# Performance work log

Hardware: AMD Instinct MI355X
Metric: run time of the kernel (lower is better)

## Reference

```python
import jax, jax.numpy as jnp
import numpy as np

NEG_SLOPE = 0.2


def gat_layer(x, src, dst, W, a_src, a_dst, b, heads, ch, concat, n_nodes):
    # x: [N, F_in], W: [F_in, heads*ch]
    h = (x @ W).reshape(n_nodes, heads, ch)              # [N, H, C]
    alpha_src = jnp.sum(h * a_src, axis=-1)              # [N, H]
    alpha_dst = jnp.sum(h * a_dst, axis=-1)              # [N, H]
    e = jax.nn.leaky_relu(alpha_src[src] + alpha_dst[dst], NEG_SLOPE)  # [E, H]
    # segment softmax over edges grouped by destination node
    e_max = jax.ops.segment_max(e, dst, num_segments=n_nodes)          # [N, H]
    ex = jnp.exp(e - e_max[dst])                                       # [E, H]
    denom = jax.ops.segment_sum(ex, dst, num_segments=n_nodes)         # [N, H]
    alpha = ex / denom[dst]                                            # [E, H]
    msg = h[src] * alpha[:, :, None]                                   # [E, H, C]
    out = jax.ops.segment_sum(msg, dst, num_segments=n_nodes)          # [N, H, C]
    if concat:
        out = out.reshape(n_nodes, heads * ch)
    else:
        out = out.mean(axis=1)
    return out + b


def setup_inputs() -> dict:
    key = jax.random.key(0)
    ks = jax.random.split(key, 16)
    N, E, F_in = 50000, 800000, 128
    H, C, OUT = 4, 32, 64
    x = jax.random.normal(ks[0], (N, F_in), dtype=jnp.float32)
    edge_index = jax.random.randint(ks[1], (2, E), 0, N, dtype=jnp.int64)
    s = 0.1
    return {
        "x": x,
        "edge_index": edge_index,
        "W1": jax.random.normal(ks[2], (F_in, H * C), dtype=jnp.float32) * s,
        "a_src1": jax.random.normal(ks[3], (H, C), dtype=jnp.float32) * s,
        "a_dst1": jax.random.normal(ks[4], (H, C), dtype=jnp.float32) * s,
        "b1": jnp.zeros((H * C,), dtype=jnp.float32),
        "W2": jax.random.normal(ks[5], (H * C, H * C), dtype=jnp.float32) * s,
        "a_src2": jax.random.normal(ks[6], (H, C), dtype=jnp.float32) * s,
        "a_dst2": jax.random.normal(ks[7], (H, C), dtype=jnp.float32) * s,
        "b2": jnp.zeros((H * C,), dtype=jnp.float32),
        "W3": jax.random.normal(ks[8], (H * C, H * OUT), dtype=jnp.float32) * s,
        "a_src3": jax.random.normal(ks[9], (H, OUT), dtype=jnp.float32) * s,
        "a_dst3": jax.random.normal(ks[10], (H, OUT), dtype=jnp.float32) * s,
        "b3": jnp.zeros((OUT,), dtype=jnp.float32),
    }


def reference(x, edge_index, W1, a_src1, a_dst1, b1, W2, a_src2, a_dst2, b2,
              W3, a_src3, a_dst3, b3):
    N = x.shape[0]
    # PyG GATConv default add_self_loops=True
    loop = jnp.arange(N, dtype=edge_index.dtype)
    src = jnp.concatenate([edge_index[0], loop])
    dst = jnp.concatenate([edge_index[1], loop])
    h = gat_layer(x, src, dst, W1, a_src1, a_dst1, b1, 4, 32, True, N)
    h = gat_layer(h, src, dst, W2, a_src2, a_dst2, b2, 4, 32, True, N)
    out = gat_layer(h, src, dst, W3, a_src3, a_dst3, b3, 4, 64, False, N)
    return out
```

## Files before the change

### kernel.cpp

```cpp
#include <hip/hip_runtime.h>
#include <hip/hip_fp16.h>

constexpr int HEADS = 4;

typedef _Float16 half8 __attribute__((ext_vector_type(8)));
typedef _Float16 half2v __attribute__((ext_vector_type(2)));
typedef float f32x4 __attribute__((ext_vector_type(4)));

__device__ __forceinline__ float lrelu(float x) { return x > 0.f ? x : 0.2f * x; }


__global__ void count_deg_kernel(const int* __restrict__ ei, int* __restrict__ deg,
                                 int E, int N) {
  int e = blockIdx.x * 256 + threadIdx.x;
  int EP = E + N;
  if (e < EP) {
    int d = (e < E) ? ei[E + e] : (e - E);
    atomicAdd(&deg[d], 1);
  }
}

__global__ void scan_block_kernel(const int* __restrict__ deg, int* __restrict__ rowp,
                                  int* __restrict__ partials, int N) {
  __shared__ int sm[1024];
  int t = threadIdx.x;
  int i = blockIdx.x * 1024 + t;
  int v = (i < N) ? deg[i] : 0;
  sm[t] = v;
  __syncthreads();
  for (int off = 1; off < 1024; off <<= 1) {
    int tmp = (t >= off) ? sm[t - off] : 0;
    __syncthreads();
    sm[t] += tmp;
    __syncthreads();
  }
  if (i < N) rowp[i] = sm[t] - v;
  if (t == 1023) partials[blockIdx.x] = sm[t];
}

__global__ void scan_partials_kernel(int* partials, int nb) {
  __shared__ int sm[1024];
  int t = threadIdx.x;
  int v = (t < nb) ? partials[t] : 0;
  sm[t] = v;
  __syncthreads();
  for (int off = 1; off < 1024; off <<= 1) {
    int tmp = (t >= off) ? sm[t - off] : 0;
    __syncthreads();
    sm[t] += tmp;
    __syncthreads();
  }
  if (t < nb) partials[t] = sm[t] - v;
}

__global__ void add_off_kernel(int* __restrict__ rowp, const int* __restrict__ partials,
                               int N, int EP) {
  int i = blockIdx.x * 256 + threadIdx.x;
  if (i < N) rowp[i] += partials[i >> 10];
  if (i == 0) rowp[N] = EP;
}

__global__ void scatter_kernel(const int* __restrict__ ei, const int* __restrict__ rowp,
                               int* __restrict__ cursor, int* __restrict__ col,
                               int* __restrict__ dstarr, int E, int N) {
  int e = blockIdx.x * 256 + threadIdx.x;
  int EP = E + N;
  if (e < EP) {
    int s, d;
    if (e < E) { s = ei[e]; d = ei[E + e]; }
    else       { s = e - E; d = e - E; }
    int pos = rowp[d] + atomicAdd(&cursor[d], 1);
    col[pos] = s;
    dstarr[pos] = d;
  }
}


__global__ void convert_wt3_kernel(const float* __restrict__ W1, _Float16* __restrict__ Wt1,
                                   const float* __restrict__ W2, _Float16* __restrict__ Wt2,
                                   const float* __restrict__ W3, _Float16* __restrict__ Wt3) {
  const float* W; _Float16* Wt; int Fout;
  if (blockIdx.y == 0)      { W = W1; Wt = Wt1; Fout = 128; }
  else if (blockIdx.y == 1) { W = W2; Wt = Wt2; Fout = 128; }
  else                      { W = W3; Wt = Wt3; Fout = 256; }
  int i = blockIdx.x * 256 + threadIdx.x;
  if (i < 128 * Fout) {
    int c = i >> 7, k = i & 127;
    Wt[c * 128 + k] = (_Float16)W[k * Fout + c];
  }
}


template <int AF32>
__global__ __launch_bounds__(256) void gemm_mfma_kernel(
    const void* __restrict__ Xv, const _Float16* __restrict__ Wt,
    _Float16* __restrict__ O, int N, int Fout) {
  const int w = threadIdx.x >> 6;
  const int lane = threadIdx.x & 63;
  const int r = lane & 15, g = lane >> 4;
  const int row0 = blockIdx.x * 64 + w * 16;
  const int colpan = blockIdx.y * 128;

  int rowl = row0 + r;
  if (rowl >= N) rowl = N - 1;

  f32x4 acc[8];
#pragma unroll
  for (int c = 0; c < 8; ++c) acc[c] = {0.f, 0.f, 0.f, 0.f};

#pragma unroll
  for (int s = 0; s < 4; ++s) {
    half8 a;
    if constexpr (AF32) {
      const float* X = (const float*)Xv;
      float4 a0 = *(const float4*)&X[(size_t)rowl * 128 + s * 32 + g * 8];
      float4 a1 = *(const float4*)&X[(size_t)rowl * 128 + s * 32 + g * 8 + 4];
      a = half8{(_Float16)a0.x, (_Float16)a0.y, (_Float16)a0.z, (_Float16)a0.w,
                (_Float16)a1.x, (_Float16)a1.y, (_Float16)a1.z, (_Float16)a1.w};
    } else {
      const _Float16* X = (const _Float16*)Xv;
      a = *(const half8*)&X[(size_t)rowl * 128 + s * 32 + g * 8];
    }
#pragma unroll
    for (int c = 0; c < 8; ++c) {
      half8 b = *(const half8*)&Wt[(size_t)(colpan + c * 16 + r) * 128 + s * 32 + g * 8];
      acc[c] = __builtin_amdgcn_mfma_f32_16x16x32_f16(a, b, acc[c], 0, 0, 0);
    }
  }

#pragma unroll
  for (int c = 0; c < 8; ++c) {
    int ocol = colpan + c * 16 + r;
#pragma unroll
    for (int q = 0; q < 4; ++q) {
      int orow = row0 + g * 4 + q;
      if (orow < N) O[(size_t)orow * Fout + ocol] = (_Float16)acc[c][q];
    }
  }
}


template <int LP>
__global__ __launch_bounds__(256) void alpha_kernel(
    const _Float16* __restrict__ H, const float* __restrict__ a_s,
    const float* __restrict__ a_d, float* __restrict__ asrc,
    float* __restrict__ adst, int N) {
  const int C = LP * 8;
  int g = blockIdx.x * 256 + threadIdx.x;
  int pair = g / LP;
  int sub = g % LP;
  if (pair >= N * 4) return;
  int h = pair & 3;
  half8 hv = *(const half8*)&H[(size_t)pair * C + sub * 8];
  float4 s0 = *(const float4*)&a_s[h * C + sub * 8];
  float4 s1 = *(const float4*)&a_s[h * C + sub * 8 + 4];
  float4 d0 = *(const float4*)&a_d[h * C + sub * 8];
  float4 d1 = *(const float4*)&a_d[h * C + sub * 8 + 4];
  float ps = (float)hv[0] * s0.x + (float)hv[1] * s0.y + (float)hv[2] * s0.z +
             (float)hv[3] * s0.w + (float)hv[4] * s1.x + (float)hv[5] * s1.y +
             (float)hv[6] * s1.z + (float)hv[7] * s1.w;
  float pd = (float)hv[0] * d0.x + (float)hv[1] * d0.y + (float)hv[2] * d0.z +
             (float)hv[3] * d0.w + (float)hv[4] * d1.x + (float)hv[5] * d1.y +
             (float)hv[6] * d1.z + (float)hv[7] * d1.w;
#pragma unroll
  for (int off = 1; off < LP; off <<= 1) {
    ps += __shfl_xor(ps, off, 64);
    pd += __shfl_xor(pd, off, 64);
  }
  if (sub == 0) { asrc[pair] = ps; adst[pair] = pd; }
}


__global__ __launch_bounds__(256) void ew_kernel(
    const int* __restrict__ col, const int* __restrict__ dstarr,
    const float* __restrict__ asrc, const float* __restrict__ adst,
    float* __restrict__ wgt, int EP) {
  int j = blockIdx.x * 256 + threadIdx.x;
  if (j < EP) {
    int s = col[j], d = dstarr[j];
    float4 a = *(const float4*)&asrc[s * 4];
    float4 b = *(const float4*)&adst[d * 4];
    float4 o;
    o.x = __expf(lrelu(a.x + b.x));
    o.y = __expf(lrelu(a.y + b.y));
    o.z = __expf(lrelu(a.z + b.z));
    o.w = __expf(lrelu(a.w + b.w));
    *(float4*)&wgt[(size_t)j * 4] = o;
  }
}


__global__ __launch_bounds__(256) void aggregate_concat_kernel(
    const _Float16* __restrict__ H, const float* __restrict__ wgt,
    const float* __restrict__ bias, const int* __restrict__ rowp,
    const int* __restrict__ col, _Float16* __restrict__ out, int N) {
  int n = blockIdx.x * 4 + (threadIdx.x >> 6);
  if (n >= N) return;
  int lane = threadIdx.x & 63;
  int h = lane >> 4;
  int j = rowp[n], end = rowp[n + 1];
  float ax = 0.f, ay = 0.f, denom = 0.f;
  for (; j + 7 < end; j += 8) {
    int s[8]; float w[8]; half2v f[8];
#pragma unroll
    for (int k = 0; k < 8; ++k) s[k] = col[j + k];
#pragma unroll
    for (int k = 0; k < 8; ++k) {
      w[k] = wgt[(size_t)(j + k) * 4 + h];
      f[k] = *(const half2v*)&H[(size_t)s[k] * 128 + lane * 2];
    }
#pragma unroll
    for (int k = 0; k < 8; ++k) {
      denom += w[k];
      ax += w[k] * (float)f[k].x;
      ay += w[k] * (float)f[k].y;
    }
  }
  for (; j < end; ++j) {
    int s0 = col[j];
    float w0 = wgt[(size_t)j * 4 + h];
    half2v f0 = *(const half2v*)&H[(size_t)s0 * 128 + lane * 2];
    denom += w0;
    ax += w0 * (float)f0.x;
    ay += w0 * (float)f0.y;
  }
  float inv = 1.f / denom;
  half2v o;
  o.x = (_Float16)(ax * inv + bias[lane * 2]);
  o.y = (_Float16)(ay * inv + bias[lane * 2 + 1]);
  *(half2v*)&out[(size_t)n * 128 + lane * 2] = o;
}


__global__ __launch_bounds__(128) void aggregate_mean_kernel(
    const _Float16* __restrict__ H, const float* __restrict__ wgt,
    const float* __restrict__ bias, const int* __restrict__ rowp,
    const int* __restrict__ col, float* __restrict__ out, int N) {
  __shared__ float2 red[128];
  int n = blockIdx.x;
  int t = threadIdx.x;
  int h = t >> 5;
  int j = rowp[n], end = rowp[n + 1];
  float ax = 0.f, ay = 0.f, denom = 0.f;
  for (; j + 7 < end; j += 8) {
    int s[8]; float w[8]; half2v f[8];
#pragma unroll
    for (int k = 0; k < 8; ++k) s[k] = col[j + k];
#pragma unroll
    for (int k = 0; k < 8; ++k) {
      w[k] = wgt[(size_t)(j + k) * 4 + h];
      f[k] = *(const half2v*)&H[(size_t)s[k] * 256 + t * 2];
    }
#pragma unroll
    for (int k = 0; k < 8; ++k) {
      denom += w[k];
      ax += w[k] * (float)f[k].x;
      ay += w[k] * (float)f[k].y;
    }
  }
  for (; j < end; ++j) {
    int s0 = col[j];
    float w0 = wgt[(size_t)j * 4 + h];
    half2v f0 = *(const half2v*)&H[(size_t)s0 * 256 + t * 2];
    denom += w0;
    ax += w0 * (float)f0.x;
    ay += w0 * (float)f0.y;
  }
  float inv = 1.f / denom;
  red[t] = make_float2(ax * inv, ay * inv);
  __syncthreads();
  if (t < 32) {
    float2 r0 = red[t], r1 = red[t + 32], r2 = red[t + 64], r3 = red[t + 96];
    float2 o = make_float2(0.25f * (r0.x + r1.x + r2.x + r3.x) + bias[t * 2],
                           0.25f * (r0.y + r1.y + r2.y + r3.y) + bias[t * 2 + 1]);
    *(float2*)&out[n * 64 + t * 2] = o;
  }
}


extern "C" void kernel_launch(void* const* d_in, const int* in_sizes, int n_in,
                              void* d_out, int out_size, void* d_ws, size_t ws_size,
                              hipStream_t stream) {
  const float* x   = (const float*)d_in[0];
  const int*   ei  = (const int*)d_in[1];
  const float* W1  = (const float*)d_in[2];
  const float* as1 = (const float*)d_in[3];
  const float* ad1 = (const float*)d_in[4];
  const float* b1  = (const float*)d_in[5];
  const float* W2  = (const float*)d_in[6];
  const float* as2 = (const float*)d_in[7];
  const float* ad2 = (const float*)d_in[8];
  const float* b2  = (const float*)d_in[9];
  const float* W3  = (const float*)d_in[10];
  const float* as3 = (const float*)d_in[11];
  const float* ad3 = (const float*)d_in[12];
  const float* b3  = (const float*)d_in[13];
  float* out = (float*)d_out;

  const int N  = in_sizes[0] / 128;
  const int E  = in_sizes[1] / 2;
  const int EP = E + N;

  char* p = (char*)d_ws;
  auto carve = [&](size_t bytes) -> void* {
    void* r = (void*)p;
    p += (bytes + 255) & ~size_t(255);
    return r;
  };
  int*      deg  = (int*)carve(size_t(N) * 4);
  int*      rowp = (int*)carve(size_t(N + 1) * 4);
  int*      cur  = (int*)carve(size_t(N) * 4);
  int*      part = (int*)carve(1024 * 4);
  int*      col  = (int*)carve(size_t(EP) * 4);
  int*      darr = (int*)carve(size_t(EP) * 4);
  float*    asrc = (float*)carve(size_t(N) * HEADS * 4);
  float*    adst = (float*)carve(size_t(N) * HEADS * 4);
  float*    wgt  = (float*)carve(size_t(EP) * HEADS * 4);
  _Float16* Wt1  = (_Float16*)carve(128 * 128 * 2);
  _Float16* Wt2  = (_Float16*)carve(128 * 128 * 2);
  _Float16* Wt3  = (_Float16*)carve(256 * 128 * 2);
  _Float16* Hb   = (_Float16*)carve(size_t(N) * 256 * 2);
  _Float16* Ab   = (_Float16*)carve(size_t(N) * 128 * 2);

  hipMemsetAsync(deg, 0, size_t(N) * 4, stream);
  hipMemsetAsync(cur, 0, size_t(N) * 4, stream);

  int gEP = (EP + 255) / 256;
  count_deg_kernel<<<gEP, 256, 0, stream>>>(ei, deg, E, N);
  int nb = (N + 1023) / 1024;
  scan_block_kernel<<<nb, 1024, 0, stream>>>(deg, rowp, part, N);
  scan_partials_kernel<<<1, 1024, 0, stream>>>(part, nb);
  add_off_kernel<<<(N + 256) / 256, 256, 0, stream>>>(rowp, part, N, EP);
  scatter_kernel<<<gEP, 256, 0, stream>>>(ei, rowp, cur, col, darr, E, N);

  convert_wt3_kernel<<<dim3(128, 3), 256, 0, stream>>>(W1, Wt1, W2, Wt2, W3, Wt3);

  int gM = (N + 63) / 64;
  int gN4 = (N + 3) / 4;
  int gA32 = (N * 4 * 4 + 255) / 256;
  int gA64 = (N * 4 * 8 + 255) / 256;

  gemm_mfma_kernel<1><<<dim3(gM, 1), 256, 0, stream>>>(x, Wt1, Hb, N, 128);
  alpha_kernel<4><<<gA32, 256, 0, stream>>>(Hb, as1, ad1, asrc, adst, N);
  ew_kernel<<<gEP, 256, 0, stream>>>(col, darr, asrc, adst, wgt, EP);
  aggregate_concat_kernel<<<gN4, 256, 0, stream>>>(Hb, wgt, b1, rowp, col, Ab, N);
  gemm_mfma_kernel<0><<<dim3(gM, 1), 256, 0, stream>>>(Ab, Wt2, Hb, N, 128);
  alpha_kernel<4><<<gA32, 256, 0, stream>>>(Hb, as2, ad2, asrc, adst, N);
  ew_kernel<<<gEP, 256, 0, stream>>>(col, darr, asrc, adst, wgt, EP);
  aggregate_concat_kernel<<<gN4, 256, 0, stream>>>(Hb, wgt, b2, rowp, col, Ab, N);
  gemm_mfma_kernel<0><<<dim3(gM, 2), 256, 0, stream>>>(Ab, Wt3, Hb, N, 256);
  alpha_kernel<8><<<gA64, 256, 0, stream>>>(Hb, as3, ad3, asrc, adst, N);
  ew_kernel<<<gEP, 256, 0, stream>>>(col, darr, asrc, adst, wgt, EP);
  aggregate_mean_kernel<<<N, 128, 0, stream>>>(Hb, wgt, b3, rowp, col, out, N);
}
```

Measured before the change: 450.1 us.

## Fuse attention logits into GEMM epilogue and edge weights into aggregation

The per-head source and destination attention scores are now computed in the MFMA GEMM epilogue with lane shuffles, which removes the separate alpha kernel and its re-read of H. The per-edge exp(leaky_relu) weights are recomputed inside the aggregation kernels from asrc/adst instead of being written to and read from a materialised edge-weight buffer. This also drops the dst array and the ew kernel. The trade is redundant exp computation per lane and extra random gathers of asrc in the aggregation, in exchange for less global memory traffic and fewer launches.

```diff
diff --git a/kernel.cpp b/kernel.cpp
--- a/kernel.cpp
+++ b/kernel.cpp
@@ -62,7 +62,7 @@
 
 __global__ void scatter_kernel(const int* __restrict__ ei, const int* __restrict__ rowp,
                                int* __restrict__ cursor, int* __restrict__ col,
-                               int* __restrict__ dstarr, int E, int N) {
+                               int E, int N) {
   int e = blockIdx.x * 256 + threadIdx.x;
   int EP = E + N;
   if (e < EP) {
@@ -71,7 +71,6 @@
     else       { s = e - E; d = e - E; }
     int pos = rowp[d] + atomicAdd(&cursor[d], 1);
     col[pos] = s;
-    dstarr[pos] = d;
   }
 }
 
@@ -91,10 +90,12 @@
 }
 
 
-template <int AF32>
+template <int AF32, int CPH>
 __global__ __launch_bounds__(256) void gemm_mfma_kernel(
     const void* __restrict__ Xv, const _Float16* __restrict__ Wt,
-    _Float16* __restrict__ O, int N, int Fout) {
+    const float* __restrict__ a_s, const float* __restrict__ a_d,
+    _Float16* __restrict__ O, float* __restrict__ asrc, float* __restrict__ adst,
+    int N, int Fout) {
   const int w = threadIdx.x >> 6;
   const int lane = threadIdx.x & 63;
   const int r = lane & 15, g = lane >> 4;
@@ -137,67 +138,64 @@
       if (orow < N) O[(size_t)orow * Fout + ocol] = (_Float16)acc[c][q];
     }
   }
-}
-
-
-template <int LP>
-__global__ __launch_bounds__(256) void alpha_kernel(
-    const _Float16* __restrict__ H, const float* __restrict__ a_s,
-    const float* __restrict__ a_d, float* __restrict__ asrc,
-    float* __restrict__ adst, int N) {
-  const int C = LP * 8;
-  int g = blockIdx.x * 256 + threadIdx.x;
-  int pair = g / LP;
-  int sub = g % LP;
-  if (pair >= N * 4) return;
-  int h = pair & 3;
-  half8 hv = *(const half8*)&H[(size_t)pair * C + sub * 8];
-  float4 s0 = *(const float4*)&a_s[h * C + sub * 8];
-  float4 s1 = *(const float4*)&a_s[h * C + sub * 8 + 4];
-  float4 d0 = *(const float4*)&a_d[h * C + sub * 8];
-  float4 d1 = *(const float4*)&a_d[h * C + sub * 8 + 4];
-  float ps = (float)hv[0] * s0.x + (float)hv[1] * s0.y + (float)hv[2] * s0.z +
-             (float)hv[3] * s0.w + (float)hv[4] * s1.x + (float)hv[5] * s1.y +
-             (float)hv[6] * s1.z + (float)hv[7] * s1.w;
-  float pd = (float)hv[0] * d0.x + (float)hv[1] * d0.y + (float)hv[2] * d0.z +
-             (float)hv[3] * d0.w + (float)hv[4] * d1.x + (float)hv[5] * d1.y +
-             (float)hv[6] * d1.z + (float)hv[7] * d1.w;
-#pragma unroll
-  for (int off = 1; off < LP; off <<= 1) {
-    ps += __shfl_xor(ps, off, 64);
-    pd += __shfl_xor(pd, off, 64);
-  }
-  if (sub == 0) { asrc[pair] = ps; adst[pair] = pd; }
-}
-
-
-__global__ __launch_bounds__(256) void ew_kernel(
-    const int* __restrict__ col, const int* __restrict__ dstarr,
-    const float* __restrict__ asrc, const float* __restrict__ adst,
-    float* __restrict__ wgt, int EP) {
-  int j = blockIdx.x * 256 + threadIdx.x;
-  if (j < EP) {
-    int s = col[j], d = dstarr[j];
-    float4 a = *(const float4*)&asrc[s * 4];
-    float4 b = *(const float4*)&adst[d * 4];
-    float4 o;
-    o.x = __expf(lrelu(a.x + b.x));
-    o.y = __expf(lrelu(a.y + b.y));
-    o.z = __expf(lrelu(a.z + b.z));
-    o.w = __expf(lrelu(a.w + b.w));
-    *(float4*)&wgt[(size_t)j * 4] = o;
+
+  constexpr int HPP = 8 / CPH;
+  constexpr int C = CPH * 16;
+  const int hbase = blockIdx.y * HPP;
+  float ps[4][HPP], pd[4][HPP];
+#pragma unroll
+  for (int q = 0; q < 4; ++q)
+#pragma unroll
+    for (int hh = 0; hh < HPP; ++hh) { ps[q][hh] = 0.f; pd[q][hh] = 0.f; }
+
+#pragma unroll
+  for (int c = 0; c < 8; ++c) {
+    int hh = c / CPH;
+    int ch = (c % CPH) * 16 + r;
+    float asv = a_s[(hbase + hh) * C + ch];
+    float adv = a_d[(hbase + hh) * C + ch];
+#pragma unroll
+    for (int q = 0; q < 4; ++q) {
+      ps[q][hh] += acc[c][q] * asv;
+      pd[q][hh] += acc[c][q] * adv;
+    }
+  }
+#pragma unroll
+  for (int m = 1; m < 16; m <<= 1) {
+#pragma unroll
+    for (int q = 0; q < 4; ++q)
+#pragma unroll
+      for (int hh = 0; hh < HPP; ++hh) {
+        ps[q][hh] += __shfl_xor(ps[q][hh], m, 64);
+        pd[q][hh] += __shfl_xor(pd[q][hh], m, 64);
+      }
+  }
+  if (r == 0) {
+#pragma unroll
+    for (int q = 0; q < 4; ++q) {
+      int row = row0 + g * 4 + q;
+      if (row < N) {
+#pragma unroll
+        for (int hh = 0; hh < HPP; ++hh) {
+          asrc[row * 4 + hbase + hh] = ps[q][hh];
+          adst[row * 4 + hbase + hh] = pd[q][hh];
+        }
+      }
+    }
   }
 }
 
 
 __global__ __launch_bounds__(256) void aggregate_concat_kernel(
-    const _Float16* __restrict__ H, const float* __restrict__ wgt,
-    const float* __restrict__ bias, const int* __restrict__ rowp,
-    const int* __restrict__ col, _Float16* __restrict__ out, int N) {
+    const _Float16* __restrict__ H, const float* __restrict__ asrc,
+    const float* __restrict__ adst, const float* __restrict__ bias,
+    const int* __restrict__ rowp, const int* __restrict__ col,
+    _Float16* __restrict__ out, int N) {
   int n = blockIdx.x * 4 + (threadIdx.x >> 6);
   if (n >= N) return;
   int lane = threadIdx.x & 63;
   int h = lane >> 4;
+  float ad = adst[n * 4 + h];
   int j = rowp[n], end = rowp[n + 1];
   float ax = 0.f, ay = 0.f, denom = 0.f;
   for (; j + 7 < end; j += 8) {
@@ -206,7 +204,7 @@
     for (int k = 0; k < 8; ++k) s[k] = col[j + k];
 #pragma unroll
     for (int k = 0; k < 8; ++k) {
-      w[k] = wgt[(size_t)(j + k) * 4 + h];
+      w[k] = __expf(lrelu(asrc[s[k] * 4 + h] + ad));
       f[k] = *(const half2v*)&H[(size_t)s[k] * 128 + lane * 2];
     }
 #pragma unroll
@@ -218,7 +216,7 @@
   }
   for (; j < end; ++j) {
     int s0 = col[j];
-    float w0 = wgt[(size_t)j * 4 + h];
+    float w0 = __expf(lrelu(asrc[s0 * 4 + h] + ad));
     half2v f0 = *(const half2v*)&H[(size_t)s0 * 128 + lane * 2];
     denom += w0;
     ax += w0 * (float)f0.x;
@@ -233,13 +231,15 @@
 
 
 __global__ __launch_bounds__(128) void aggregate_mean_kernel(
-    const _Float16* __restrict__ H, const float* __restrict__ wgt,
-    const float* __restrict__ bias, const int* __restrict__ rowp,
-    const int* __restrict__ col, float* __restrict__ out, int N) {
+    const _Float16* __restrict__ H, const float* __restrict__ asrc,
+    const float* __restrict__ adst, const float* __restrict__ bias,
+    const int* __restrict__ rowp, const int* __restrict__ col,
+    float* __restrict__ out, int N) {
   __shared__ float2 red[128];
   int n = blockIdx.x;
   int t = threadIdx.x;
   int h = t >> 5;
+  float ad = adst[n * 4 + h];
   int j = rowp[n], end = rowp[n + 1];
   float ax = 0.f, ay = 0.f, denom = 0.f;
   for (; j + 7 < end; j += 8) {
@@ -248,7 +248,7 @@
     for (int k = 0; k < 8; ++k) s[k] = col[j + k];
 #pragma unroll
     for (int k = 0; k < 8; ++k) {
-      w[k] = wgt[(size_t)(j + k) * 4 + h];
+      w[k] = __expf(lrelu(asrc[s[k] * 4 + h] + ad));
       f[k] = *(const half2v*)&H[(size_t)s[k] * 256 + t * 2];
     }
 #pragma unroll
@@ -260,7 +260,7 @@
   }
   for (; j < end; ++j) {
     int s0 = col[j];
-    float w0 = wgt[(size_t)j * 4 + h];
+    float w0 = __expf(lrelu(asrc[s0 * 4 + h] + ad));
     half2v f0 = *(const half2v*)&H[(size_t)s0 * 256 + t * 2];
     denom += w0;
     ax += w0 * (float)f0.x;
@@ -312,10 +312,8 @@
   int*      cur  = (int*)carve(size_t(N) * 4);
   int*      part = (int*)carve(1024 * 4);
   int*      col  = (int*)carve(size_t(EP) * 4);
-  int*      darr = (int*)carve(size_t(EP) * 4);
   float*    asrc = (float*)carve(size_t(N) * HEADS * 4);
   float*    adst = (float*)carve(size_t(N) * HEADS * 4);
-  float*    wgt  = (float*)carve(size_t(EP) * HEADS * 4);
   _Float16* Wt1  = (_Float16*)carve(128 * 128 * 2);
   _Float16* Wt2  = (_Float16*)carve(128 * 128 * 2);
   _Float16* Wt3  = (_Float16*)carve(256 * 128 * 2);
@@ -331,25 +329,20 @@
   scan_block_kernel<<<nb, 1024, 0, stream>>>(deg, rowp, part, N);
   scan_partials_kernel<<<1, 1024, 0, stream>>>(part, nb);
   add_off_kernel<<<(N + 256) / 256, 256, 0, stream>>>(rowp, part, N, EP);
-  scatter_kernel<<<gEP, 256, 0, stream>>>(ei, rowp, cur, col, darr, E, N);
+  scatter_kernel<<<gEP, 256, 0, stream>>>(ei, rowp, cur, col, E, N);
 
   convert_wt3_kernel<<<dim3(128, 3), 256, 0, stream>>>(W1, Wt1, W2, Wt2, W3, Wt3);
 
   int gM = (N + 63) / 64;
   int gN4 = (N + 3) / 4;
-  int gA32 = (N * 4 * 4 + 255) / 256;
-  int gA64 = (N * 4 * 8 + 255) / 256;
-
-  gemm_mfma_kernel<1><<<dim3(gM, 1), 256, 0, stream>>>(x, Wt1, Hb, N, 128);
-  alpha_kernel<4><<<gA32, 256, 0, stream>>>(Hb, as1, ad1, asrc, adst, N);
-  ew_kernel<<<gEP, 256, 0, stream>>>(col, darr, asrc, adst, wgt, EP);
-  aggregate_concat_kernel<<<gN4, 256, 0, stream>>>(Hb, wgt, b1, rowp, col, Ab, N);
-  gemm_mfma_kernel<0><<<dim3(gM, 1), 256, 0, stream>>>(Ab, Wt2, Hb, N, 128);
-  alpha_kernel<4><<<gA32, 256, 0, stream>>>(Hb, as2, ad2, asrc, adst, N);
-  ew_kernel<<<gEP, 256, 0, stream>>>(col, darr, asrc, adst, wgt, EP);
-  aggregate_concat_kernel<<<gN4, 256, 0, stream>>>(Hb, wgt, b2, rowp, col, Ab, N);
-  gemm_mfma_kernel<0><<<dim3(gM, 2), 256, 0, stream>>>(Ab, Wt3, Hb, N, 256);
-  alpha_kernel<8><<<gA64, 256, 0, stream>>>(Hb, as3, ad3, asrc, adst, N);
-  ew_kernel<<<gEP, 256, 0, stream>>>(col, darr, asrc, adst, wgt, EP);
-  aggregate_mean_kernel<<<N, 128, 0, stream>>>(Hb, wgt, b3, rowp, col, out, N);
-}
+
+  gemm_mfma_kernel<1, 2><<<dim3(gM, 1), 256, 0, stream>>>(
+      x, Wt1, as1, ad1, Hb, asrc, adst, N, 128);
+  aggregate_concat_kernel<<<gN4, 256, 0, stream>>>(Hb, asrc, adst, b1, rowp, col, Ab, N);
+  gemm_mfma_kernel<0, 2><<<dim3(gM, 1), 256, 0, stream>>>(
+      Ab, Wt2, as2, ad2, Hb, asrc, adst, N, 128);
+  aggregate_concat_kernel<<<gN4, 256, 0, stream>>>(Hb, asrc, adst, b2, rowp, col, Ab, N);
+  gemm_mfma_kernel<0, 4><<<dim3(gM, 2), 256, 0, stream>>>(
+      Ab, Wt3, as3, ad3, Hb, asrc, adst, N, 256);
+  aggregate_mean_kernel<<<N, 128, 0, stream>>>(Hb, asrc, adst, b3, rowp, col, out, N);
+}
```

Result: faster. 422.5 us (-6.1%).
